# Kernel optimization log

Measured on AMD Instinct MI355X. Metric: run time of the kernel, lower is better.

## Reference

```python
import jax, jax.numpy as jnp
import numpy as np
import math

SQRT2 = math.sqrt(2.0)
SQRT_2PI = math.sqrt(2.0 * math.pi)
T = 1.0


def _margin_from_bn(xt_flat):
    # xt_flat: [B, C*L]. torch .std() is unbiased (ddof=1).
    std = jnp.abs(jnp.std(xt_flat, axis=1, ddof=1))  # [B]
    mean = jnp.mean(xt_flat, axis=1)                  # [B]
    z = -mean / std
    cdf = 0.5 * (1.0 + jax.lax.erf(z / SQRT2))        # norm.cdf(-mean/std)
    safe_cdf = jnp.maximum(cdf, 1e-30)                # guard div; branch selected by where
    margin_a = -std * jnp.exp(-(mean / std) ** 2 / 2.0) / SQRT_2PI / safe_cdf + mean
    margin = jnp.where(cdf > 0.001, margin_a, -3.0 * std)
    # original detaches margin (computed on CPU via numpy/scipy)
    return jax.lax.stop_gradient(margin)


def reference(x_s, x_t, x_ts, x_st, i):
    B, C = x_ts.shape[0], x_ts.shape[1]
    xs = x_ts.reshape(B, C, -1)  # source: [B, C, L]
    xt = x_st.reshape(B, C, -1)  # target: [B, C, L]
    margin = _margin_from_bn(xt.reshape(B, -1))  # [B]
    # distillation_loss(source=xs, target=xt, T, dims=1, margin)
    target = jnp.maximum(xt / T, margin[:, None, None])
    entropy = jax.nn.softmax(xs / T, axis=1) * jax.nn.log_softmax(target / T, axis=1)
    channel_entropy = -jnp.sum(entropy, axis=1)          # [B, L]
    batch_mean_entropy = jnp.mean(channel_entropy, axis=1)  # [B]
    loss = jnp.mean(batch_mean_entropy)
    return (loss, entropy)


def setup_inputs() -> dict:
    key = jax.random.key(0)
    k1, k2, k3, k4 = jax.random.split(key, 4)
    return {
        "x_s": jax.random.normal(k1, (1,), dtype=jnp.float32),
        "x_t": jax.random.normal(k2, (1,), dtype=jnp.float32),
        "x_ts": jax.random.normal(k3, (8, 1024, 64, 64), dtype=jnp.float32),
        "x_st": jax.random.normal(k4, (8, 1024, 64, 64), dtype=jnp.float32),
        "i": 0,
    }
```

## Files before the change

### kernel.cpp

```cpp
#include <hip/hip_runtime.h>
#include <math.h>

#define BB 8
#define CC 1024
#define LL 4096
#define NPB (CC*LL)
#define TOTAL (BB*CC*LL)


__global__ void k_batch_sums(const float* __restrict__ xt, double* __restrict__ sums) {
    int b = blockIdx.y;
    const float4* p = (const float4*)(xt + (size_t)b * NPB);
    int t = blockIdx.x * blockDim.x + threadIdx.x;
    double s1 = 0.0, s2 = 0.0;
    #pragma unroll
    for (int j4 = 0; j4 < 4; ++j4) {
        float4 v[4];
        #pragma unroll
        for (int k = 0; k < 4; ++k) v[k] = p[(size_t)(j4 * 4 + k) * 65536 + t];
        #pragma unroll
        for (int k = 0; k < 4; ++k) {
            float q1 = (v[k].x + v[k].y) + (v[k].z + v[k].w);
            float q2 = (v[k].x * v[k].x + v[k].y * v[k].y)
                     + (v[k].z * v[k].z + v[k].w * v[k].w);
            s1 += (double)q1;
            s2 += (double)q2;
        }
    }
    for (int off = 32; off; off >>= 1) {
        s1 += __shfl_down(s1, off, 64);
        s2 += __shfl_down(s2, off, 64);
    }
    __shared__ double ls1[4], ls2[4];
    int lane = threadIdx.x & 63, w = threadIdx.x >> 6;
    if (lane == 0) { ls1[w] = s1; ls2[w] = s2; }
    __syncthreads();
    if (threadIdx.x == 0) {
        atomicAdd(&sums[2 * b],     ls1[0] + ls1[1] + ls1[2] + ls1[3]);
        atomicAdd(&sums[2 * b + 1], ls2[0] + ls2[1] + ls2[2] + ls2[3]);
    }
}

__global__ void k_margin(const double* __restrict__ sums, float* __restrict__ margin) {
    int b = threadIdx.x;
    if (b < BB) {
        double n = (double)NPB;
        double s1 = sums[2 * b], s2 = sums[2 * b + 1];
        double mean = s1 / n;
        double var = (s2 - s1 * s1 / n) / (n - 1.0);
        double sd = sqrt(var);
        double z = -mean / sd;
        double cdf = 0.5 * (1.0 + erf(z / 1.4142135623730951));
        double safe = fmax(cdf, 1e-30);
        double r = mean / sd;
        double ma = -sd * exp(-r * r * 0.5) / 2.5066282746310002 / safe + mean;
        double m = (cdf > 0.001) ? ma : -3.0 * sd;
        margin[b] = (float)m;
    }
}

__global__ void k_colstats(const float* __restrict__ xs, const float* __restrict__ xt,
                           const float* __restrict__ margin,
                           float* __restrict__ ssA, float* __restrict__ syA) {
    int lane = threadIdx.x & 63, w = threadIdx.x >> 6;
    int l0 = blockIdx.x * 256 + lane * 4;
    int b = blockIdx.y;
    int c0 = blockIdx.z * 64 + w;
    float mg = margin[b];
    const float* ps = xs + (size_t)b * NPB + l0;
    const float* pt = xt + (size_t)b * NPB + l0;
    float ss[4] = {0, 0, 0, 0}, sy[4] = {0, 0, 0, 0};
    #pragma unroll
    for (int j4 = 0; j4 < 4; ++j4) {
        float4 vs[4], vt[4];
        #pragma unroll
        for (int k = 0; k < 4; ++k) {
            int c = c0 + 4 * (j4 * 4 + k);
            vs[k] = *(const float4*)(ps + (size_t)c * LL);
            vt[k] = *(const float4*)(pt + (size_t)c * LL);
        }
        #pragma unroll
        for (int k = 0; k < 4; ++k) {
            ss[0] += __expf(vs[k].x); ss[1] += __expf(vs[k].y);
            ss[2] += __expf(vs[k].z); ss[3] += __expf(vs[k].w);
            sy[0] += __expf(fmaxf(vt[k].x, mg)); sy[1] += __expf(fmaxf(vt[k].y, mg));
            sy[2] += __expf(fmaxf(vt[k].z, mg)); sy[3] += __expf(fmaxf(vt[k].w, mg));
        }
    }
    __shared__ float red[4][64][8];
    #pragma unroll
    for (int k = 0; k < 4; ++k) { red[w][lane][k] = ss[k]; red[w][lane][4 + k] = sy[k]; }
    __syncthreads();
    if (w == 0) {
        #pragma unroll
        for (int k = 0; k < 4; ++k) {
            float vss = red[0][lane][k] + red[1][lane][k] + red[2][lane][k] + red[3][lane][k];
            float vsy = red[0][lane][4+k] + red[1][lane][4+k] + red[2][lane][4+k] + red[3][lane][4+k];
            atomicAdd(&ssA[b * LL + l0 + k], vss);
            atomicAdd(&syA[b * LL + l0 + k], vsy);
        }
    }
}

__global__ void k_entropy(const float* __restrict__ xs, const float* __restrict__ xt,
                          const float* __restrict__ margin,
                          const float* __restrict__ ssA, const float* __restrict__ syA,
                          float* __restrict__ out1, double* __restrict__ lossAcc) {
    int lane = threadIdx.x & 63, w = threadIdx.x >> 6;
    int l0 = blockIdx.x * 256 + lane * 4;
    int b = blockIdx.y;
    int c0 = blockIdx.z * 64 + w;
    float mg = margin[b];
    float4 ssv = *(const float4*)(ssA + b * LL + l0);
    float4 syv = *(const float4*)(syA + b * LL + l0);
    float A0 = __logf(ssv.x), A1 = __logf(ssv.y), A2 = __logf(ssv.z), A3 = __logf(ssv.w);
    float B0 = __logf(syv.x), B1 = __logf(syv.y), B2 = __logf(syv.z), B3 = __logf(syv.w);
    const float* ps = xs + (size_t)b * NPB + l0;
    const float* pt = xt + (size_t)b * NPB + l0;
    float* po = out1 + (size_t)b * NPB + l0;
    float acc = 0.f;
    #pragma unroll
    for (int j4 = 0; j4 < 4; ++j4) {
        float4 vs[4], vt[4];
        int cbase = c0 + 4 * (j4 * 4);
        #pragma unroll
        for (int k = 0; k < 4; ++k) {
            int c = cbase + 4 * k;
            vs[k] = *(const float4*)(ps + (size_t)c * LL);
            vt[k] = *(const float4*)(pt + (size_t)c * LL);
        }
        #pragma unroll
        for (int k = 0; k < 4; ++k) {
            int c = cbase + 4 * k;
            float4 e;
            e.x = __expf(vs[k].x - A0) * (fmaxf(vt[k].x, mg) - B0);
            e.y = __expf(vs[k].y - A1) * (fmaxf(vt[k].y, mg) - B1);
            e.z = __expf(vs[k].z - A2) * (fmaxf(vt[k].z, mg) - B2);
            e.w = __expf(vs[k].w - A3) * (fmaxf(vt[k].w, mg) - B3);
            *(float4*)(po + (size_t)c * LL) = e;
            acc += (e.x + e.y) + (e.z + e.w);
        }
    }
    for (int off = 32; off; off >>= 1) acc += __shfl_down(acc, off, 64);
    __shared__ float wacc[4];
    if (lane == 0) wacc[w] = acc;
    __syncthreads();
    if (threadIdx.x == 0) {
        double t = (double)wacc[0] + wacc[1] + wacc[2] + wacc[3];
        atomicAdd(lossAcc, t);
    }
}

__global__ void k_finalize(const double* __restrict__ lossAcc, float* __restrict__ out) {
    if (threadIdx.x == 0) out[0] = (float)(-lossAcc[0] / (double)(BB * LL));
}

extern "C" void kernel_launch(void* const* d_in, const int* in_sizes, int n_in,
                              void* d_out, int out_size, void* d_ws, size_t ws_size,
                              hipStream_t stream) {
    const float* x_ts = (const float*)d_in[2];
    const float* x_st = (const float*)d_in[3];
    float* out = (float*)d_out;

    double* sums    = (double*)d_ws;
    double* lossAcc = (double*)((char*)d_ws + 128);
    float*  margins = (float*)((char*)d_ws + 192);
    float*  ssA     = (float*)((char*)d_ws + 256);
    float*  syA     = (float*)((char*)d_ws + 256 + 131072);

    hipMemsetAsync(d_ws, 0, 256 + 262144, stream);

    k_batch_sums<<<dim3(256, BB), 256, 0, stream>>>(x_st, sums);
    k_margin<<<1, 64, 0, stream>>>(sums, margins);
    k_colstats<<<dim3(16, BB, 16), 256, 0, stream>>>(x_ts, x_st, margins, ssA, syA);
    k_entropy<<<dim3(16, BB, 16), 256, 0, stream>>>(x_ts, x_st, margins, ssA, syA,
                                                    out + 1, lossAcc);
    k_finalize<<<1, 64, 0, stream>>>(lossAcc, out);
}
```

Before: 393.6 us.

## Fuse margin, column softmax stats and entropy into one register-resident kernel

Merges the margin computation, per-column exp-sum reduction and entropy write into a single kernel where each 1024-thread block owns 32 columns across all 1024 channels. Values are kept in registers between the reduction and output phases, so xs and xt are read once instead of twice, and the global atomic column buffers and their memset go away. The trade-off is 1024-thread blocks with high register use and narrow 128-byte row segments per access, which may reduce occupancy or DRAM efficiency.

```diff
diff --git a/kernel.cpp b/kernel.cpp
--- a/kernel.cpp
+++ b/kernel.cpp
@@ -5,7 +5,7 @@
 #define CC 1024
 #define LL 4096
 #define NPB (CC*LL)
-#define TOTAL (BB*CC*LL)
+#define LT 32
 
 
 __global__ void k_batch_sums(const float* __restrict__ xt, double* __restrict__ sums) {
@@ -41,9 +41,24 @@
     }
 }
 
-__global__ void k_margin(const double* __restrict__ sums, float* __restrict__ margin) {
-    int b = threadIdx.x;
-    if (b < BB) {
+__global__ __launch_bounds__(1024)
+void k_fused(const float* __restrict__ xs, const float* __restrict__ xt,
+             const double* __restrict__ sums,
+             float* __restrict__ out1, double* __restrict__ lossAcc) {
+    int tid = threadIdx.x;
+    int b = blockIdx.y;
+    int L0 = blockIdx.x * LT;
+    int q = tid & 7;
+    int g = tid >> 3;
+    int lane = tid & 63, w = tid >> 6;
+
+    __shared__ float s_mg;
+    __shared__ __align__(16) float s_red[2][16][8][4];
+    __shared__ __align__(16) float s_sinv[8][4];
+    __shared__ __align__(16) float s_blog[8][4];
+    __shared__ float wacc[16];
+
+    if (tid == 0) {
         double n = (double)NPB;
         double s1 = sums[2 * b], s2 = sums[2 * b + 1];
         double mean = s1 / n;
@@ -54,99 +69,80 @@
         double safe = fmax(cdf, 1e-30);
         double r = mean / sd;
         double ma = -sd * exp(-r * r * 0.5) / 2.5066282746310002 / safe + mean;
-        double m = (cdf > 0.001) ? ma : -3.0 * sd;
-        margin[b] = (float)m;
+        s_mg = (float)((cdf > 0.001) ? ma : -3.0 * sd);
     }
-}
+    __syncthreads();
+    float mg = s_mg;
 
-__global__ void k_colstats(const float* __restrict__ xs, const float* __restrict__ xt,
-                           const float* __restrict__ margin,
-                           float* __restrict__ ssA, float* __restrict__ syA) {
-    int lane = threadIdx.x & 63, w = threadIdx.x >> 6;
-    int l0 = blockIdx.x * 256 + lane * 4;
-    int b = blockIdx.y;
-    int c0 = blockIdx.z * 64 + w;
-    float mg = margin[b];
-    const float* ps = xs + (size_t)b * NPB + l0;
-    const float* pt = xt + (size_t)b * NPB + l0;
+    const float* ps = xs + (size_t)b * NPB + L0 + q * 4;
+    const float* pt = xt + (size_t)b * NPB + L0 + q * 4;
+
+    float4 es[8], yv[8];
     float ss[4] = {0, 0, 0, 0}, sy[4] = {0, 0, 0, 0};
     #pragma unroll
-    for (int j4 = 0; j4 < 4; ++j4) {
-        float4 vs[4], vt[4];
+    for (int i = 0; i < 8; ++i) {
+        size_t off = (size_t)(g + 128 * i) * LL;
+        float4 s4 = *(const float4*)(ps + off);
+        float4 t4 = *(const float4*)(pt + off);
+        float4 e, y;
+        e.x = __expf(s4.x); e.y = __expf(s4.y); e.z = __expf(s4.z); e.w = __expf(s4.w);
+        y.x = fmaxf(t4.x, mg); y.y = fmaxf(t4.y, mg);
+        y.z = fmaxf(t4.z, mg); y.w = fmaxf(t4.w, mg);
+        es[i] = e; yv[i] = y;
+        ss[0] += e.x; ss[1] += e.y; ss[2] += e.z; ss[3] += e.w;
+        sy[0] += __expf(y.x); sy[1] += __expf(y.y);
+        sy[2] += __expf(y.z); sy[3] += __expf(y.w);
+    }
+    #pragma unroll
+    for (int off = 8; off < 64; off <<= 1) {
         #pragma unroll
         for (int k = 0; k < 4; ++k) {
-            int c = c0 + 4 * (j4 * 4 + k);
-            vs[k] = *(const float4*)(ps + (size_t)c * LL);
-            vt[k] = *(const float4*)(pt + (size_t)c * LL);
+            ss[k] += __shfl_xor(ss[k], off, 64);
+            sy[k] += __shfl_xor(sy[k], off, 64);
         }
+    }
+    if (lane < 8) {
         #pragma unroll
         for (int k = 0; k < 4; ++k) {
-            ss[0] += __expf(vs[k].x); ss[1] += __expf(vs[k].y);
-            ss[2] += __expf(vs[k].z); ss[3] += __expf(vs[k].w);
-            sy[0] += __expf(fmaxf(vt[k].x, mg)); sy[1] += __expf(fmaxf(vt[k].y, mg));
-            sy[2] += __expf(fmaxf(vt[k].z, mg)); sy[3] += __expf(fmaxf(vt[k].w, mg));
+            s_red[0][w][lane][k] = ss[k];
+            s_red[1][w][lane][k] = sy[k];
         }
     }
-    __shared__ float red[4][64][8];
-    #pragma unroll
-    for (int k = 0; k < 4; ++k) { red[w][lane][k] = ss[k]; red[w][lane][4 + k] = sy[k]; }
     __syncthreads();
-    if (w == 0) {
+    if (tid < 64) {
+        int a  = tid >> 5;
+        int qq = (tid >> 2) & 7;
+        int k  = tid & 3;
+        float t = 0.f;
         #pragma unroll
-        for (int k = 0; k < 4; ++k) {
-            float vss = red[0][lane][k] + red[1][lane][k] + red[2][lane][k] + red[3][lane][k];
-            float vsy = red[0][lane][4+k] + red[1][lane][4+k] + red[2][lane][4+k] + red[3][lane][4+k];
-            atomicAdd(&ssA[b * LL + l0 + k], vss);
-            atomicAdd(&syA[b * LL + l0 + k], vsy);
-        }
+        for (int ww = 0; ww < 16; ++ww) t += s_red[a][ww][qq][k];
+        if (a == 0) s_sinv[qq][k] = 1.0f / t;
+        else        s_blog[qq][k] = __logf(t);
     }
-}
+    __syncthreads();
+    float4 sinv = *(const float4*)&s_sinv[q][0];
+    float4 blog = *(const float4*)&s_blog[q][0];
 
-__global__ void k_entropy(const float* __restrict__ xs, const float* __restrict__ xt,
-                          const float* __restrict__ margin,
-                          const float* __restrict__ ssA, const float* __restrict__ syA,
-                          float* __restrict__ out1, double* __restrict__ lossAcc) {
-    int lane = threadIdx.x & 63, w = threadIdx.x >> 6;
-    int l0 = blockIdx.x * 256 + lane * 4;
-    int b = blockIdx.y;
-    int c0 = blockIdx.z * 64 + w;
-    float mg = margin[b];
-    float4 ssv = *(const float4*)(ssA + b * LL + l0);
-    float4 syv = *(const float4*)(syA + b * LL + l0);
-    float A0 = __logf(ssv.x), A1 = __logf(ssv.y), A2 = __logf(ssv.z), A3 = __logf(ssv.w);
-    float B0 = __logf(syv.x), B1 = __logf(syv.y), B2 = __logf(syv.z), B3 = __logf(syv.w);
-    const float* ps = xs + (size_t)b * NPB + l0;
-    const float* pt = xt + (size_t)b * NPB + l0;
-    float* po = out1 + (size_t)b * NPB + l0;
+    float* po = out1 + (size_t)b * NPB + L0 + q * 4;
     float acc = 0.f;
     #pragma unroll
-    for (int j4 = 0; j4 < 4; ++j4) {
-        float4 vs[4], vt[4];
-        int cbase = c0 + 4 * (j4 * 4);
-        #pragma unroll
-        for (int k = 0; k < 4; ++k) {
-            int c = cbase + 4 * k;
-            vs[k] = *(const float4*)(ps + (size_t)c * LL);
-            vt[k] = *(const float4*)(pt + (size_t)c * LL);
-        }
-        #pragma unroll
-        for (int k = 0; k < 4; ++k) {
-            int c = cbase + 4 * k;
-            float4 e;
-            e.x = __expf(vs[k].x - A0) * (fmaxf(vt[k].x, mg) - B0);
-            e.y = __expf(vs[k].y - A1) * (fmaxf(vt[k].y, mg) - B1);
-            e.z = __expf(vs[k].z - A2) * (fmaxf(vt[k].z, mg) - B2);
-            e.w = __expf(vs[k].w - A3) * (fmaxf(vt[k].w, mg) - B3);
-            *(float4*)(po + (size_t)c * LL) = e;
-            acc += (e.x + e.y) + (e.z + e.w);
-        }
+    for (int i = 0; i < 8; ++i) {
+        size_t off = (size_t)(g + 128 * i) * LL;
+        float4 e;
+        e.x = es[i].x * sinv.x * (yv[i].x - blog.x);
+        e.y = es[i].y * sinv.y * (yv[i].y - blog.y);
+        e.z = es[i].z * sinv.z * (yv[i].z - blog.z);
+        e.w = es[i].w * sinv.w * (yv[i].w - blog.w);
+        *(float4*)(po + off) = e;
+        acc += (e.x + e.y) + (e.z + e.w);
     }
     for (int off = 32; off; off >>= 1) acc += __shfl_down(acc, off, 64);
-    __shared__ float wacc[4];
     if (lane == 0) wacc[w] = acc;
     __syncthreads();
-    if (threadIdx.x == 0) {
-        double t = (double)wacc[0] + wacc[1] + wacc[2] + wacc[3];
+    if (tid == 0) {
+        double t = 0.0;
+        #pragma unroll
+        for (int ww = 0; ww < 16; ++ww) t += (double)wacc[ww];
         atomicAdd(lossAcc, t);
     }
 }
@@ -164,16 +160,10 @@
 
     double* sums    = (double*)d_ws;
     double* lossAcc = (double*)((char*)d_ws + 128);
-    float*  margins = (float*)((char*)d_ws + 192);
-    float*  ssA     = (float*)((char*)d_ws + 256);
-    float*  syA     = (float*)((char*)d_ws + 256 + 131072);
 
-    hipMemsetAsync(d_ws, 0, 256 + 262144, stream);
+    hipMemsetAsync(d_ws, 0, 256, stream);
 
     k_batch_sums<<<dim3(256, BB), 256, 0, stream>>>(x_st, sums);
-    k_margin<<<1, 64, 0, stream>>>(sums, margins);
-    k_colstats<<<dim3(16, BB, 16), 256, 0, stream>>>(x_ts, x_st, margins, ssA, syA);
-    k_entropy<<<dim3(16, BB, 16), 256, 0, stream>>>(x_ts, x_st, margins, ssA, syA,
-                                                    out + 1, lossAcc);
+    k_fused<<<dim3(LL / LT, BB), 1024, 0, stream>>>(x_ts, x_st, sums, out + 1, lossAcc);
     k_finalize<<<1, 64, 0, stream>>>(lossAcc, out);
 }
```

Result: no change. 391.6 us (-0.5%).
